# Optimization experiments

Measured on AMD Instinct MI355X. Metric: run time of the kernel, lower is better.

Reference implementation:

```python
import jax, jax.numpy as jnp
import numpy as np

D_EMBED = 768
N_HEADS = 12
HEAD_DIM = D_EMBED // N_HEADS


def setup_inputs() -> dict:
    key = jax.random.key(0)
    ks = jax.random.split(key, 9)
    B, T, C = 4, 2048, D_EMBED
    s = 1.0 / np.sqrt(C)
    return {
        "x": jax.random.normal(ks[0], (B, T, C), dtype=jnp.float32),
        "Wq": jax.random.normal(ks[1], (C, C), dtype=jnp.float32) * s,
        "bq": jnp.zeros((C,), dtype=jnp.float32),
        "Wk": jax.random.normal(ks[2], (C, C), dtype=jnp.float32) * s,
        "bk": jnp.zeros((C,), dtype=jnp.float32),
        "Wv": jax.random.normal(ks[3], (C, C), dtype=jnp.float32) * s,
        "bv": jnp.zeros((C,), dtype=jnp.float32),
        "Wo": jax.random.normal(ks[4], (C, C), dtype=jnp.float32) * s,
        "bo": jnp.zeros((C,), dtype=jnp.float32),
    }


def reference(x, Wq, bq, Wk, bk, Wv, bv, Wo, bo):
    B, T, C = x.shape
    H, D = N_HEADS, HEAD_DIM
    # projections -> [B, H, T, D]
    q = (x @ Wq + bq).reshape(B, T, H, D).transpose(0, 2, 1, 3)
    k = (x @ Wk + bk).reshape(B, T, H, D).transpose(0, 2, 1, 3)
    v = (x @ Wv + bv).reshape(B, T, H, D).transpose(0, 2, 1, 3)
    # full attention matrix [B, H, T, T] (faithful to manual implementation)
    scores = jnp.einsum('bhqd,bhkd->bhqk', q, k) / jnp.sqrt(jnp.float32(D))
    causal = jnp.tril(jnp.ones((T, T), dtype=bool))
    scores = jnp.where(causal, scores, jnp.float32(-jnp.inf))
    weights = jax.nn.softmax(scores, axis=-1)
    out = jnp.einsum('bhqk,bhkd->bhqd', weights, v)
    out = out.transpose(0, 2, 1, 3).reshape(B, T, C)
    return out @ Wo + bo
```

## Files before the change

kernel.cpp:

```cpp
#include <hip/hip_runtime.h>

#define T_LEN 2048
#define C_DIM 768
#define NH 12
#define HD 64
#define B_SZ 4
#define M_ROWS (B_SZ * T_LEN)
#define WSZ (C_DIM * C_DIM)
#define CH 520

typedef __bf16 bf16x8 __attribute__((ext_vector_type(8)));
typedef float f32x4 __attribute__((ext_vector_type(4)));
typedef float f32x16 __attribute__((ext_vector_type(16)));

__device__ __forceinline__ unsigned short f2bf(float f) {
    union { __bf16 b; unsigned short u; } c;
    c.b = (__bf16)f;
    return c.u;
}

__device__ __forceinline__ float fast_exp2(float x) {
    float r;
    asm("v_exp_f32 %0, %1" : "=v"(r) : "v"(x));
    return r;
}

__device__ __forceinline__ unsigned cvt_pk_bf16(float a, float b) {
    unsigned r;
    asm("v_cvt_pk_bf16_f32 %0, %1, %2" : "=v"(r) : "v"(a), "v"(b));
    return r;
}

__device__ __forceinline__ void perml32_swap(unsigned& a, unsigned& b) {
    asm("v_permlane32_swap_b32 %0, %1" : "+v"(a), "+v"(b));
}

__device__ __forceinline__ void gl2lds16(const void* g, void* l) {
    __builtin_amdgcn_global_load_lds(
        (const __attribute__((address_space(1))) unsigned int*)g,
        (__attribute__((address_space(3))) unsigned int*)l, 16, 0, 0);
}

__global__ __launch_bounds__(256) void conv_x(const float* __restrict__ x,
                                              unsigned short* __restrict__ xb)
{
    const int i = blockIdx.x * 256 + threadIdx.x;
    float4 v = ((const float4*)x)[i];
    ushort4 o;
    o.x = f2bf(v.x); o.y = f2bf(v.y); o.z = f2bf(v.z); o.w = f2bf(v.w);
    ((ushort4*)xb)[i] = o;
}

__global__ __launch_bounds__(256) void conv_wt(
    const float* __restrict__ W0, const float* __restrict__ W1,
    const float* __restrict__ W2, const float* __restrict__ W3,
    unsigned short* __restrict__ WtAll)
{
    __shared__ float tile[32][33];
    const int z = blockIdx.z;
    const float* W = (z == 0) ? W0 : (z == 1) ? W1 : (z == 2) ? W2 : W3;
    unsigned short* out = WtAll + (size_t)z * WSZ;
    const int k0 = blockIdx.x * 32, n0 = blockIdx.y * 32;
    const int r = threadIdx.x >> 3, c4 = (threadIdx.x & 7) * 4;
    float4 v = *(const float4*)&W[(size_t)(k0 + r) * C_DIM + n0 + c4];
    tile[r][c4 + 0] = v.x;
    tile[r][c4 + 1] = v.y;
    tile[r][c4 + 2] = v.z;
    tile[r][c4 + 3] = v.w;
    __syncthreads();
    ushort4 o;
    o.x = f2bf(tile[c4 + 0][r]);
    o.y = f2bf(tile[c4 + 1][r]);
    o.z = f2bf(tile[c4 + 2][r]);
    o.w = f2bf(tile[c4 + 3][r]);
    *(ushort4*)&out[(size_t)(n0 + r) * C_DIM + k0 + c4] = o;
}

template <int BN, int MODE>
__global__ __launch_bounds__(256, 2) void gemm_tile(
    const unsigned short* __restrict__ A, const unsigned short* __restrict__ Wt,
    const float* __restrict__ b0, const float* __restrict__ b1,
    const float* __restrict__ b2,
    unsigned short* __restrict__ qg, unsigned short* __restrict__ kg,
    unsigned short* __restrict__ vtg, float* __restrict__ outF)
{
    constexpr int NFC = BN / 32;
    constexpr int NY = (MODE == 0 ? 2304 : 768) / BN;
    __shared__ __align__(16) unsigned short As[2][128 * 64];
    __shared__ __align__(16) unsigned short Bs[2][BN * 64];

    const int tid = threadIdx.x;
    const int lane = tid & 63, w = tid >> 6;
    const int L15 = lane & 15, quad = lane >> 4;
    const int wm = w >> 1, wn = w & 1;

    const int raw = blockIdx.x;
    const int xcd = raw & 7, i = raw >> 3;
    const int mx = xcd * 8 + i / NY;
    const int ny = i % NY;

    const int lr = lane >> 3;
    const int lg8 = (lane & 7) ^ lr;
    const size_t aBase = (size_t)(mx * 128 + w * 8 + lr) * C_DIM + lg8 * 8;
    const size_t bBase = (size_t)(ny * BN + w * 8 + lr) * C_DIM + lg8 * 8;

    auto stage = [&](int kt, int buf) {
        const size_t ko = (size_t)kt * 64;
#pragma unroll
        for (int c = 0; c < 4; c++)
            gl2lds16(&A[aBase + (size_t)c * 32 * C_DIM + ko],
                     &As[buf][(c * 32 + w * 8) * 64]);
#pragma unroll
        for (int c = 0; c < BN / 32; c++)
            gl2lds16(&Wt[bBase + (size_t)c * 32 * C_DIM + ko],
                     &Bs[buf][(c * 32 + w * 8) * 64]);
    };

    const int sg0 = (quad ^ (L15 & 7)) * 16;
    const int sg1 = ((4 + quad) ^ (L15 & 7)) * 16;
    const int aRowB = (wm * 64 + L15) * 128;
    const int bRowB = (wn * (BN / 2) + L15) * 128;

    f32x4 acc[4][NFC];
#pragma unroll
    for (int fr = 0; fr < 4; fr++)
#pragma unroll
        for (int fc = 0; fc < NFC; fc++) acc[fr][fc] = 0.0f;

    stage(0, 0);
    __syncthreads();

    for (int kt = 0; kt < 12; kt++) {
        const int cur = kt & 1;
        if (kt < 11) stage(kt + 1, cur ^ 1);
        const char* Ac = (const char*)As[cur];
        const char* Bc = (const char*)Bs[cur];
        bf16x8 av[4][2], bv[NFC][2];
#pragma unroll
        for (int fr = 0; fr < 4; fr++)
#pragma unroll
            for (int kh = 0; kh < 2; kh++)
                av[fr][kh] = *(const bf16x8*)(Ac + aRowB + fr * 2048 + (kh ? sg1 : sg0));
#pragma unroll
        for (int fc = 0; fc < NFC; fc++)
#pragma unroll
            for (int kh = 0; kh < 2; kh++)
                bv[fc][kh] = *(const bf16x8*)(Bc + bRowB + fc * 2048 + (kh ? sg1 : sg0));
        __builtin_amdgcn_s_setprio(1);
#pragma unroll
        for (int fr = 0; fr < 4; fr++)
#pragma unroll
            for (int fc = 0; fc < NFC; fc++)
#pragma unroll
                for (int kh = 0; kh < 2; kh++)
                    acc[fr][fc] = __builtin_amdgcn_mfma_f32_16x16x32_bf16(
                        av[fr][kh], bv[fc][kh], acc[fr][fc], 0, 0, 0);
        __builtin_amdgcn_s_setprio(0);
        __syncthreads();
    }

    if (MODE == 0) {
        const int z = (ny * BN) / 768;
        const float* bias = (z == 0) ? b0 : (z == 1) ? b1 : b2;
        const float qs = (z == 0) ? 0.18033688011112042f : 1.0f;
#pragma unroll
        for (int fc = 0; fc < NFC; fc++) {
            const int n = ny * BN + wn * (BN / 2) + fc * 16 + L15;
            const int nl = n - z * 768;
            const int h = nl >> 6, d = nl & 63;
            const float bn = bias[nl];
#pragma unroll
            for (int fr = 0; fr < 4; fr++) {
                const int mB = mx * 128 + wm * 64 + fr * 16 + quad * 4;
                const int b = mB >> 11, tB = mB & (T_LEN - 1);
                if (z < 2) {
                    unsigned short* o = z ? kg : qg;
#pragma unroll
                    for (int r = 0; r < 4; r++)
                        o[(((size_t)(b * NH + h)) * T_LEN + tB + r) * HD + d] =
                            f2bf((acc[fr][fc][r] + bn) * qs);
                } else {
                    ushort4 o4;
                    o4.x = f2bf(acc[fr][fc][0] + bn);
                    o4.y = f2bf(acc[fr][fc][1] + bn);
                    o4.z = f2bf(acc[fr][fc][2] + bn);
                    o4.w = f2bf(acc[fr][fc][3] + bn);
                    *(ushort4*)&vtg[(((size_t)(b * NH + h)) * HD + d) * T_LEN + tB] = o4;
                }
            }
        }
    } else {
#pragma unroll
        for (int fc = 0; fc < NFC; fc++) {
            const int n = ny * BN + wn * (BN / 2) + fc * 16 + L15;
            const float bn = b0[n];
#pragma unroll
            for (int fr = 0; fr < 4; fr++) {
                const int mB = mx * 128 + wm * 64 + fr * 16 + quad * 4;
#pragma unroll
                for (int r = 0; r < 4; r++)
                    outF[(size_t)(mB + r) * C_DIM + n] = acc[fr][fc][r] + bn;
            }
        }
    }
}

__global__ __launch_bounds__(256, 4) void attn_mfma(
    const unsigned short* __restrict__ qg, const unsigned short* __restrict__ kg,
    const unsigned short* __restrict__ vtg, unsigned short* __restrict__ attb)
{
    __shared__ __align__(16) unsigned short Ks[2][8 * CH];
    __shared__ __align__(16) unsigned short Vs[2][8 * CH];
    const int tid = threadIdx.x;
    const int lane = tid & 63, w = tid >> 6;
    const int L15 = lane & 15, L31 = lane & 31;
    const int quad = lane >> 4, r4 = (lane >> 4) & 1, r5 = lane >> 5;

    const int n = blockIdx.x;
    const int bh = n % (B_SZ * NH);
    const int m = n / (B_SZ * NH);
    const int qi = (m & 1) ? (m >> 1) : (15 - (m >> 1));
    const size_t base = (size_t)bh * T_LEN * HD;
    const int q0 = qi * 128;
    const int nk = 2 * qi + 2;
    const int qrow = q0 + w * 32 + L31;

    bf16x8 qf[4];
#pragma unroll
    for (int kc = 0; kc < 4; kc++)
        qf[kc] = *(const bf16x8*)&qg[base + (size_t)qrow * HD + kc * 16 + r5 * 8];

    f32x16 accO[2];
#pragma unroll
    for (int md = 0; md < 2; md++) accO[md] = 0.0f;
    f32x4 lacc = 0.0f;

    auto stage = [&](int kt, int buf) {
        const int ktb = kt * 64;
        gl2lds16(&kg[base + (size_t)(ktb + w * 16 + L15) * HD + quad * 8],
                 &Ks[buf][(2 * w) * CH]);
        gl2lds16(&kg[base + (size_t)(ktb + w * 16 + L15) * HD + 32 + quad * 8],
                 &Ks[buf][(2 * w + 1) * CH]);
        gl2lds16(&vtg[base + (size_t)(w * 16 + L15) * T_LEN + ktb + quad * 8],
                 &Vs[buf][(2 * w) * CH]);
        gl2lds16(&vtg[base + (size_t)(w * 16 + L15) * T_LEN + ktb + 32 + quad * 8],
                 &Vs[buf][(2 * w + 1) * CH]);
    };

    stage(0, 0);
    __syncthreads();

    const int qmaxw = q0 + w * 32 + 31;
    const int qminw = q0 + w * 32;

    for (int kt = 0; kt < nk; kt++) {
        const int cur = kt & 1;
        if (kt + 1 < nk) stage(kt + 1, cur ^ 1);
        const int ktb = kt * 64;
        if (ktb <= qmaxw) {
            f32x16 sa[2];
#pragma unroll
            for (int mi = 0; mi < 2; mi++) {
                sa[mi] = 0.0f;
#pragma unroll
                for (int kc = 0; kc < 4; kc++) {
                    const int ck = mi * 4 + r4 * 2 + (kc >> 1);
                    const int slot = L15 + 16 * ((kc & 1) * 2 + r5);
                    bf16x8 kf = *(const bf16x8*)&Ks[cur][ck * CH + slot * 8];
                    sa[mi] = __builtin_amdgcn_mfma_f32_32x32x16_bf16(
                        kf, qf[kc], sa[mi], 0, 0, 0);
                }
            }
            const bool needmask = (ktb + 63 > qminw);
            bf16x8 pfrag[4];
#pragma unroll
            for (int mi = 0; mi < 2; mi++) {
                float e[16];
#pragma unroll
                for (int g = 0; g < 4; g++) {
#pragma unroll
                    for (int rr = 0; rr < 4; rr++) {
                        float s = sa[mi][g * 4 + rr];
                        if (needmask) {
                            const int key = ktb + mi * 32 + 8 * g + 4 * r5 + rr;
                            s = (key <= qrow) ? s : -1e30f;
                        }
                        e[g * 4 + rr] = fast_exp2(s);
                        lacc[rr] += e[g * 4 + rr];
                    }
                }
#pragma unroll
                for (int h = 0; h < 2; h++) {
                    unsigned a0 = cvt_pk_bf16(e[8 * h + 0], e[8 * h + 1]);
                    unsigned a1 = cvt_pk_bf16(e[8 * h + 2], e[8 * h + 3]);
                    unsigned b0 = cvt_pk_bf16(e[8 * h + 4], e[8 * h + 5]);
                    unsigned b1 = cvt_pk_bf16(e[8 * h + 6], e[8 * h + 7]);
                    perml32_swap(a0, b0);
                    perml32_swap(a1, b1);
                    union { unsigned u[4]; bf16x8 v; } pf;
                    pf.u[0] = a0; pf.u[1] = a1; pf.u[2] = b0; pf.u[3] = b1;
                    pfrag[2 * mi + h] = pf.v;
                }
            }
#pragma unroll
            for (int md = 0; md < 2; md++) {
#pragma unroll
                for (int kc = 0; kc < 4; kc++) {
                    const int cv = md * 4 + r4 * 2 + (kc >> 1);
                    const int slot = L15 + 16 * ((kc & 1) * 2 + r5);
                    bf16x8 vf = *(const bf16x8*)&Vs[cur][cv * CH + slot * 8];
                    accO[md] = __builtin_amdgcn_mfma_f32_32x32x16_bf16(
                        vf, pfrag[kc], accO[md], 0, 0, 0);
                }
            }
        }
        __syncthreads();
    }

    const float l = (lacc[0] + lacc[1]) + (lacc[2] + lacc[3]);
    const float lt = l + __shfl_xor(l, 32, 64);
    const float inv = __builtin_amdgcn_rcpf(lt);
    const int b = bh / NH, h = bh % NH;
    const size_t orow = ((size_t)(b * T_LEN + qrow)) * C_DIM + h * HD;
#pragma unroll
    for (int md = 0; md < 2; md++) {
#pragma unroll
        for (int g = 0; g < 4; g++) {
            uint2 wv;
            wv.x = (unsigned)f2bf(accO[md][g * 4 + 0] * inv) |
                   ((unsigned)f2bf(accO[md][g * 4 + 1] * inv) << 16);
            wv.y = (unsigned)f2bf(accO[md][g * 4 + 2] * inv) |
                   ((unsigned)f2bf(accO[md][g * 4 + 3] * inv) << 16);
            *(uint2*)&attb[orow + md * 32 + 8 * g + 4 * r5] = wv;
        }
    }
}

extern "C" void kernel_launch(void* const* d_in, const int* in_sizes, int n_in,
                              void* d_out, int out_size, void* d_ws, size_t ws_size,
                              hipStream_t stream)
{
    const float* x  = (const float*)d_in[0];
    const float* Wq = (const float*)d_in[1];
    const float* bq = (const float*)d_in[2];
    const float* Wk = (const float*)d_in[3];
    const float* bk = (const float*)d_in[4];
    const float* Wv = (const float*)d_in[5];
    const float* bv = (const float*)d_in[6];
    const float* Wo = (const float*)d_in[7];
    const float* bo = (const float*)d_in[8];
    float* out = (float*)d_out;

    const size_t nMC = (size_t)M_ROWS * C_DIM;
    unsigned short* xb   = (unsigned short*)d_ws;
    unsigned short* Wt   = xb + nMC;
    unsigned short* qg   = Wt + 4 * (size_t)WSZ;
    unsigned short* kg   = qg + nMC;
    unsigned short* vtg  = kg + nMC;
    unsigned short* attb = vtg + nMC;

    conv_x<<<(int)(nMC / 1024), 256, 0, stream>>>(x, xb);
    conv_wt<<<dim3(24, 24, 4), 256, 0, stream>>>(Wq, Wk, Wv, Wo, Wt);
    gemm_tile<192, 0><<<768, 256, 0, stream>>>(xb, Wt, bq, bk, bv,
                                               qg, kg, vtg, nullptr);
    attn_mfma<<<16 * B_SZ * NH, 256, 0, stream>>>(qg, kg, vtg, attb);
    gemm_tile<96, 1><<<512, 256, 0, stream>>>(attb, Wt + 3 * (size_t)WSZ,
                                              bo, bo, bo, nullptr, nullptr,
                                              nullptr, out);
}
```

Measured before the change: 213.0 us.

## Load K/V fragments directly from global memory, dropping LDS staging and barriers

The attention kernel stops staging K and V tiles into double-buffered shared memory and instead has each wave read its MFMA operand fragments straight from global memory, relying on L1/L2 caches. This removes the LDS writes, the per-iteration __syncthreads, and the shared-memory footprint, and lets each wave exit its key loop independently once it passes the causal boundary. In exchange, the four waves of a block now each fetch the same K/V data separately through the cache hierarchy with less coalesced access, and there is no explicit prefetch overlapping loads with compute. Launch bounds are lowered from 4 to 3 blocks per SIMD target, giving the compiler more registers.

New measurement: 278.5 us. 1.31x slower.

```diff
diff --git a/kernel.cpp b/kernel.cpp
--- a/kernel.cpp
+++ b/kernel.cpp
@@ -7,7 +7,6 @@
 #define B_SZ 4
 #define M_ROWS (B_SZ * T_LEN)
 #define WSZ (C_DIM * C_DIM)
-#define CH 520
 
 typedef __bf16 bf16x8 __attribute__((ext_vector_type(8)));
 typedef float f32x4 __attribute__((ext_vector_type(4)));
@@ -205,16 +204,13 @@
     }
 }
 
-__global__ __launch_bounds__(256, 4) void attn_mfma(
+__global__ __launch_bounds__(256, 3) void attn_mfma(
     const unsigned short* __restrict__ qg, const unsigned short* __restrict__ kg,
     const unsigned short* __restrict__ vtg, unsigned short* __restrict__ attb)
 {
-    __shared__ __align__(16) unsigned short Ks[2][8 * CH];
-    __shared__ __align__(16) unsigned short Vs[2][8 * CH];
     const int tid = threadIdx.x;
     const int lane = tid & 63, w = tid >> 6;
-    const int L15 = lane & 15, L31 = lane & 31;
-    const int quad = lane >> 4, r4 = (lane >> 4) & 1, r5 = lane >> 5;
+    const int L31 = lane & 31, r5 = lane >> 5;
 
     const int n = blockIdx.x;
     const int bh = n % (B_SZ * NH);
@@ -230,91 +226,73 @@
     for (int kc = 0; kc < 4; kc++)
         qf[kc] = *(const bf16x8*)&qg[base + (size_t)qrow * HD + kc * 16 + r5 * 8];
 
+    const unsigned short* Krow = kg + base + (size_t)L31 * HD;
+    const unsigned short* Vrow = vtg + base + (size_t)L31 * T_LEN;
+
     f32x16 accO[2];
 #pragma unroll
     for (int md = 0; md < 2; md++) accO[md] = 0.0f;
     f32x4 lacc = 0.0f;
 
-    auto stage = [&](int kt, int buf) {
-        const int ktb = kt * 64;
-        gl2lds16(&kg[base + (size_t)(ktb + w * 16 + L15) * HD + quad * 8],
-                 &Ks[buf][(2 * w) * CH]);
-        gl2lds16(&kg[base + (size_t)(ktb + w * 16 + L15) * HD + 32 + quad * 8],
-                 &Ks[buf][(2 * w + 1) * CH]);
-        gl2lds16(&vtg[base + (size_t)(w * 16 + L15) * T_LEN + ktb + quad * 8],
-                 &Vs[buf][(2 * w) * CH]);
-        gl2lds16(&vtg[base + (size_t)(w * 16 + L15) * T_LEN + ktb + 32 + quad * 8],
-                 &Vs[buf][(2 * w + 1) * CH]);
-    };
-
-    stage(0, 0);
-    __syncthreads();
-
     const int qmaxw = q0 + w * 32 + 31;
     const int qminw = q0 + w * 32;
 
     for (int kt = 0; kt < nk; kt++) {
-        const int cur = kt & 1;
-        if (kt + 1 < nk) stage(kt + 1, cur ^ 1);
         const int ktb = kt * 64;
-        if (ktb <= qmaxw) {
-            f32x16 sa[2];
-#pragma unroll
-            for (int mi = 0; mi < 2; mi++) {
-                sa[mi] = 0.0f;
-#pragma unroll
-                for (int kc = 0; kc < 4; kc++) {
-                    const int ck = mi * 4 + r4 * 2 + (kc >> 1);
-                    const int slot = L15 + 16 * ((kc & 1) * 2 + r5);
-                    bf16x8 kf = *(const bf16x8*)&Ks[cur][ck * CH + slot * 8];
-                    sa[mi] = __builtin_amdgcn_mfma_f32_32x32x16_bf16(
-                        kf, qf[kc], sa[mi], 0, 0, 0);
+        if (ktb > qmaxw) break;
+        f32x16 sa[2];
+#pragma unroll
+        for (int mi = 0; mi < 2; mi++) {
+            sa[mi] = 0.0f;
+#pragma unroll
+            for (int kc = 0; kc < 4; kc++) {
+                bf16x8 kf = *(const bf16x8*)&Krow[(size_t)(ktb + mi * 32) * HD +
+                                                  kc * 16 + r5 * 8];
+                sa[mi] = __builtin_amdgcn_mfma_f32_32x32x16_bf16(
+                    kf, qf[kc], sa[mi], 0, 0, 0);
+            }
+        }
+        const bool needmask = (ktb + 63 > qminw);
+        bf16x8 pfrag[4];
+#pragma unroll
+        for (int mi = 0; mi < 2; mi++) {
+            float e[16];
+#pragma unroll
+            for (int g = 0; g < 4; g++) {
+#pragma unroll
+                for (int rr = 0; rr < 4; rr++) {
+                    float s = sa[mi][g * 4 + rr];
+                    if (needmask) {
+                        const int key = ktb + mi * 32 + 8 * g + 4 * r5 + rr;
+                        s = (key <= qrow) ? s : -1e30f;
+                    }
+                    e[g * 4 + rr] = fast_exp2(s);
+                    lacc[rr] += e[g * 4 + rr];
                 }
             }
-            const bool needmask = (ktb + 63 > qminw);
-            bf16x8 pfrag[4];
-#pragma unroll
-            for (int mi = 0; mi < 2; mi++) {
-                float e[16];
-#pragma unroll
-                for (int g = 0; g < 4; g++) {
-#pragma unroll
-                    for (int rr = 0; rr < 4; rr++) {
-                        float s = sa[mi][g * 4 + rr];
-                        if (needmask) {
-                            const int key = ktb + mi * 32 + 8 * g + 4 * r5 + rr;
-                            s = (key <= qrow) ? s : -1e30f;
-                        }
-                        e[g * 4 + rr] = fast_exp2(s);
-                        lacc[rr] += e[g * 4 + rr];
-                    }
-                }
-#pragma unroll
-                for (int h = 0; h < 2; h++) {
-                    unsigned a0 = cvt_pk_bf16(e[8 * h + 0], e[8 * h + 1]);
-                    unsigned a1 = cvt_pk_bf16(e[8 * h + 2], e[8 * h + 3]);
-                    unsigned b0 = cvt_pk_bf16(e[8 * h + 4], e[8 * h + 5]);
-                    unsigned b1 = cvt_pk_bf16(e[8 * h + 6], e[8 * h + 7]);
-                    perml32_swap(a0, b0);
-                    perml32_swap(a1, b1);
-                    union { unsigned u[4]; bf16x8 v; } pf;
-                    pf.u[0] = a0; pf.u[1] = a1; pf.u[2] = b0; pf.u[3] = b1;
-                    pfrag[2 * mi + h] = pf.v;
-                }
-            }
-#pragma unroll
-            for (int md = 0; md < 2; md++) {
-#pragma unroll
-                for (int kc = 0; kc < 4; kc++) {
-                    const int cv = md * 4 + r4 * 2 + (kc >> 1);
-                    const int slot = L15 + 16 * ((kc & 1) * 2 + r5);
-                    bf16x8 vf = *(const bf16x8*)&Vs[cur][cv * CH + slot * 8];
-                    accO[md] = __builtin_amdgcn_mfma_f32_32x32x16_bf16(
-                        vf, pfrag[kc], accO[md], 0, 0, 0);
-                }
-            }
-        }
-        __syncthreads();
+#pragma unroll
+            for (int h = 0; h < 2; h++) {
+                unsigned a0 = cvt_pk_bf16(e[8 * h + 0], e[8 * h + 1]);
+                unsigned a1 = cvt_pk_bf16(e[8 * h + 2], e[8 * h + 3]);
+                unsigned b0 = cvt_pk_bf16(e[8 * h + 4], e[8 * h + 5]);
+                unsigned b1 = cvt_pk_bf16(e[8 * h + 6], e[8 * h + 7]);
+                perml32_swap(a0, b0);
+                perml32_swap(a1, b1);
+                union { unsigned u[4]; bf16x8 v; } pf;
+                pf.u[0] = a0; pf.u[1] = a1; pf.u[2] = b0; pf.u[3] = b1;
+                pfrag[2 * mi + h] = pf.v;
+            }
+        }
+#pragma unroll
+        for (int md = 0; md < 2; md++) {
+#pragma unroll
+            for (int kc = 0; kc < 4; kc++) {
+                bf16x8 vf = *(const bf16x8*)&Vrow[(size_t)(md * 32) * T_LEN +
+                                                  ktb + kc * 16 + r5 * 8];
+                accO[md] = __builtin_amdgcn_mfma_f32_32x32x16_bf16(
+                    vf, pfrag[kc], accO[md], 0, 0, 0);
+            }
+        }
     }
 
     const float l = (lacc[0] + lacc[1]) + (lacc[2] + lacc[3]);
```

## Split long causal attention strips into two KV segments with a combine kernel

Applied to the files above, without the earlier changes.

Replaces the per-query-tile attention grid with a table-driven schedule of 24 work units per batch-head. The eight longest query strips are split into two KV-range halves, and each half writes unnormalized fp32 partial outputs and row sums to scratch. A new combine kernel adds the halves, normalizes and writes bf16. The aim is to balance causal work across workgroups and shorten the tail, at the cost of an extra launch and scratch traffic. The scratch reuses the output buffer and the x-bf16 workspace, and this appears to rely on the absence of max-subtraction in the softmax.

New measurement: 206.3 us. -3.2%, faster.

```diff
diff --git a/kernel.cpp b/kernel.cpp
--- a/kernel.cpp
+++ b/kernel.cpp
@@ -205,10 +205,18 @@
     }
 }
 
-__global__ __launch_bounds__(256, 4) void attn_mfma(
+__global__ __launch_bounds__(256, 4) void attn_part(
     const unsigned short* __restrict__ qg, const unsigned short* __restrict__ kg,
-    const unsigned short* __restrict__ vtg, unsigned short* __restrict__ attb)
-{
+    const unsigned short* __restrict__ vtg, unsigned short* __restrict__ attb,
+    float* __restrict__ pO, float* __restrict__ pL)
+{
+    static const unsigned char Uqs[24] = {15,15,7,14,14,6,13,13,12,12,5,11,
+                                          11,10,10,4,9,9,8,8,3,2,1,0};
+    static const unsigned char Uk0[24] = {0,16,0,0,15,0,0,14,0,13,0,0,
+                                          12,0,11,0,0,10,0,9,0,0,0,0};
+    static const unsigned char Uk1[24] = {16,32,16,15,30,14,14,28,13,26,12,12,
+                                          24,11,22,10,10,20,9,18,8,6,4,2};
+
     __shared__ __align__(16) unsigned short Ks[2][8 * CH];
     __shared__ __align__(16) unsigned short Vs[2][8 * CH];
     const int tid = threadIdx.x;
@@ -218,11 +226,11 @@
 
     const int n = blockIdx.x;
     const int bh = n % (B_SZ * NH);
-    const int m = n / (B_SZ * NH);
-    const int qi = (m & 1) ? (m >> 1) : (15 - (m >> 1));
+    const int u = n / (B_SZ * NH);
+    const int qs = Uqs[u];
+    const int k0 = Uk0[u], k1 = Uk1[u];
     const size_t base = (size_t)bh * T_LEN * HD;
-    const int q0 = qi * 128;
-    const int nk = 2 * qi + 2;
+    const int q0 = qs * 128;
     const int qrow = q0 + w * 32 + L31;
 
     bf16x8 qf[4];
@@ -247,15 +255,15 @@
                  &Vs[buf][(2 * w + 1) * CH]);
     };
 
-    stage(0, 0);
+    stage(k0, 0);
     __syncthreads();
 
     const int qmaxw = q0 + w * 32 + 31;
     const int qminw = q0 + w * 32;
 
-    for (int kt = 0; kt < nk; kt++) {
-        const int cur = kt & 1;
-        if (kt + 1 < nk) stage(kt + 1, cur ^ 1);
+    for (int kt = k0; kt < k1; kt++) {
+        const int cur = (kt - k0) & 1;
+        if (kt + 1 < k1) stage(kt + 1, cur ^ 1);
         const int ktb = kt * 64;
         if (ktb <= qmaxw) {
             f32x16 sa[2];
@@ -318,22 +326,78 @@
     }
 
     const float l = (lacc[0] + lacc[1]) + (lacc[2] + lacc[3]);
+    const bool split = (k0 != 0) || (k1 != 2 * qs + 2);
+    if (!split) {
+        const float lt = l + __shfl_xor(l, 32, 64);
+        const float inv = __builtin_amdgcn_rcpf(lt);
+        const int b = bh / NH, h = bh % NH;
+        const size_t orow = ((size_t)(b * T_LEN + qrow)) * C_DIM + h * HD;
+#pragma unroll
+        for (int md = 0; md < 2; md++) {
+#pragma unroll
+            for (int g = 0; g < 4; g++) {
+                uint2 wv;
+                wv.x = (unsigned)f2bf(accO[md][g * 4 + 0] * inv) |
+                       ((unsigned)f2bf(accO[md][g * 4 + 1] * inv) << 16);
+                wv.y = (unsigned)f2bf(accO[md][g * 4 + 2] * inv) |
+                       ((unsigned)f2bf(accO[md][g * 4 + 3] * inv) << 16);
+                *(uint2*)&attb[orow + md * 32 + 8 * g + 4 * r5] = wv;
+            }
+        }
+    } else {
+        const int strip = bh * 8 + (qs - 8);
+        const int seg = (k0 != 0) ? 1 : 0;
+        float4* pO4 = (float4*)pO;
+        const size_t pbase = ((size_t)(strip * 2 + seg) * 4 + w) * 512 + lane;
+#pragma unroll
+        for (int md = 0; md < 2; md++)
+#pragma unroll
+            for (int g = 0; g < 4; g++) {
+                float4 v4;
+                v4.x = accO[md][g * 4 + 0];
+                v4.y = accO[md][g * 4 + 1];
+                v4.z = accO[md][g * 4 + 2];
+                v4.w = accO[md][g * 4 + 3];
+                pO4[pbase + (size_t)(md * 4 + g) * 64] = v4;
+            }
+        pL[(size_t)(strip * 2 + seg) * 256 + w * 64 + lane] = l;
+    }
+}
+
+__global__ __launch_bounds__(256) void attn_comb(
+    const float* __restrict__ pO, const float* __restrict__ pL,
+    unsigned short* __restrict__ attb)
+{
+    const int g = blockIdx.x * 256 + threadIdx.x;
+    const int lane = g & 63, w = (g >> 6) & 3, strip = g >> 8;
+    const int r5 = lane >> 5, L31 = lane & 31;
+    const int bh = strip >> 3, qs = 8 + (strip & 7);
+
+    const float4* pO4 = (const float4*)pO;
+    const size_t b0 = ((size_t)(strip * 2 + 0) * 4 + w) * 512 + lane;
+    const size_t b1 = ((size_t)(strip * 2 + 1) * 4 + w) * 512 + lane;
+    const float l = pL[(size_t)(strip * 2 + 0) * 256 + w * 64 + lane] +
+                    pL[(size_t)(strip * 2 + 1) * 256 + w * 64 + lane];
     const float lt = l + __shfl_xor(l, 32, 64);
     const float inv = __builtin_amdgcn_rcpf(lt);
+
+    const int qrow = qs * 128 + w * 32 + L31;
     const int b = bh / NH, h = bh % NH;
     const size_t orow = ((size_t)(b * T_LEN + qrow)) * C_DIM + h * HD;
 #pragma unroll
-    for (int md = 0; md < 2; md++) {
-#pragma unroll
-        for (int g = 0; g < 4; g++) {
+    for (int md = 0; md < 2; md++)
+#pragma unroll
+        for (int gq = 0; gq < 4; gq++) {
+            const size_t e = (size_t)(md * 4 + gq) * 64;
+            float4 v1 = pO4[b0 + e];
+            float4 v2 = pO4[b1 + e];
             uint2 wv;
-            wv.x = (unsigned)f2bf(accO[md][g * 4 + 0] * inv) |
-                   ((unsigned)f2bf(accO[md][g * 4 + 1] * inv) << 16);
-            wv.y = (unsigned)f2bf(accO[md][g * 4 + 2] * inv) |
-                   ((unsigned)f2bf(accO[md][g * 4 + 3] * inv) << 16);
-            *(uint2*)&attb[orow + md * 32 + 8 * g + 4 * r5] = wv;
+            wv.x = (unsigned)f2bf((v1.x + v2.x) * inv) |
+                   ((unsigned)f2bf((v1.y + v2.y) * inv) << 16);
+            wv.y = (unsigned)f2bf((v1.z + v2.z) * inv) |
+                   ((unsigned)f2bf((v1.w + v2.w) * inv) << 16);
+            *(uint2*)&attb[orow + md * 32 + 8 * gq + 4 * r5] = wv;
         }
-    }
 }
 
 extern "C" void kernel_launch(void* const* d_in, const int* in_sizes, int n_in,
@@ -358,12 +422,15 @@
     unsigned short* kg   = qg + nMC;
     unsigned short* vtg  = kg + nMC;
     unsigned short* attb = vtg + nMC;
+    float* pO = out;
+    float* pL = (float*)xb;
 
     conv_x<<<(int)(nMC / 1024), 256, 0, stream>>>(x, xb);
     conv_wt<<<dim3(24, 24, 4), 256, 0, stream>>>(Wq, Wk, Wv, Wo, Wt);
     gemm_tile<192, 0><<<768, 256, 0, stream>>>(xb, Wt, bq, bk, bv,
                                                qg, kg, vtg, nullptr);
-    attn_mfma<<<16 * B_SZ * NH, 256, 0, stream>>>(qg, kg, vtg, attb);
+    attn_part<<<24 * B_SZ * NH, 256, 0, stream>>>(qg, kg, vtg, attb, pO, pL);
+    attn_comb<<<384, 256, 0, stream>>>(pO, pL, attb);
     gemm_tile<96, 1><<<512, 256, 0, stream>>>(attb, Wt + 3 * (size_t)WSZ,
                                               bo, bo, bo, nullptr, nullptr,
                                               nullptr, out);
```
